# Kernel optimization log

Hardware: AMD Instinct MI355X
Metric: run time of the kernel (lower is better)

## Reference

```python
import jax, jax.numpy as jnp
from jax import lax
import numpy as np

T, B, H, D = 1024, 32, 8, 32
YD = 3 * D + 1
IN = H * D


def setup_inputs() -> dict:
    key = jax.random.key(0)
    ks = jax.random.split(key, 6)
    std = 1.0 / np.sqrt(D)
    return {
        "h": jax.random.normal(ks[0], (T, B, IN), jnp.float32),
        "W_y": (jax.random.normal(ks[1], (1, H, D, YD), jnp.float32) * std),
        "W_q": (jax.random.normal(ks[2], (1, H, D, D), jnp.float32) * std),
        "W_k": (jax.random.normal(ks[3], (1, H, D, D), jnp.float32) * std),
        "w_b": (jax.random.normal(ks[4], (1, H, D, 4), jnp.float32) * std),
        "W_out": (jax.random.normal(ks[5], (IN, IN), jnp.float32) / np.sqrt(IN)),
        "state_W_y": jnp.zeros((B, H, D, YD), jnp.float32),
        "state_W_q": jnp.zeros((B, H, D, D), jnp.float32),
        "state_W_k": jnp.zeros((B, H, D, D), jnp.float32),
        "state_w_b": jnp.zeros((B, H, D, 4), jnp.float32),
        "fast_weights": jnp.zeros((B, H, D, D), jnp.float32),
    }


def _srwm(x, Wy0, Wq0, Wk0, wb0):
    # Self-referential weight matrix (self_ref_v1): x time-major (T,B,H,D).
    def step(carry, x_t):
        Wy, Wq, Wk, wb = carry
        y = jnp.einsum('bhd,bhde->bhe', x_t, Wy)                      # output with W_{t-1}
        q = jax.nn.softmax(jnp.einsum('bhd,bhde->bhe', x_t, Wq), -1)
        k = jax.nn.softmax(jnp.einsum('bhd,bhde->bhe', x_t, Wk), -1)
        beta = jax.nn.sigmoid(jnp.einsum('bhd,bhde->bhe', x_t, wb))   # (B,H,4) learning rates
        def upd(M, b_i):
            vq = jnp.einsum('bhd,bhde->bhe', q, M)
            vk = jnp.einsum('bhd,bhde->bhe', k, M)
            return M + b_i[..., None, None] * k[..., :, None] * (vq - vk)[..., None, :]
        Wy = upd(Wy, beta[..., 0])
        Wq = upd(Wq, beta[..., 1])
        Wk = upd(Wk, beta[..., 2])
        wb = upd(wb, beta[..., 3])
        return (Wy, Wq, Wk, wb), y

    _, ys = lax.scan(step, (Wy0, Wq0, Wk0, wb0), x)
    return ys  # (T,B,H,YD)


def _fast_weight_memory(q, k, v, beta, F0):
    # Delta-rule fast weight memory; q,k,v (T,B,H,D), beta (T,B,H,1), F0 (B,H,D,D).
    def step(F, qkvb):
        q_t, k_t, v_t, b_t = qkvb
        v_old = jnp.einsum('bhd,bhde->bhe', k_t, F)
        F = F + b_t[..., None] * k_t[..., :, None] * (v_t - v_old)[..., None, :]
        out_t = jnp.einsum('bhd,bhde->bhe', q_t, F)
        return F, out_t

    F_fin, out = lax.scan(step, F0, (q, k, v, beta))
    return out, F_fin  # out: (T,B,H,D)


def reference(h, W_y, W_q, W_k, w_b, W_out,
              state_W_y, state_W_q, state_W_k, state_w_b, fast_weights):
    x = jax.nn.softmax(h.reshape(T, B, H, D), axis=-1)   # phi(x)
    Wy0 = state_W_y + W_y
    Wq0 = state_W_q + W_q
    Wk0 = state_W_k + W_k
    wb0 = state_w_b + w_b
    fast_qkvb = _srwm(x, Wy0, Wq0, Wk0, wb0)             # (T,B,H,3D+1)
    fq, fk, fv, fb = jnp.split(fast_qkvb, (D, 2 * D, 3 * D), axis=-1)
    fq = jax.nn.softmax(fq, -1)
    fk = jax.nn.softmax(fk, -1)
    fb = jax.nn.sigmoid(fb)
    out, _ = _fast_weight_memory(fq, fk, fv, fb, fast_weights)
    out = out.reshape(T, B, H * D)
    out = out @ W_out.T                                  # out_linear (no bias), dropout=0
    return h + out
```

## Files before the change

kernel.cpp:

```cpp
#include <hip/hip_runtime.h>
#include <cstdint>

#define TT  1024
#define BB  32
#define HH  8
#define DD  32
#define YDN 97
#define INN 256
#define BH  (BB*HH)

typedef float v2f __attribute__((ext_vector_type(2)));
typedef float v4f __attribute__((ext_vector_type(4)));

#define PK(acc, a, b) (acc) = __builtin_elementwise_fma((a), (b), (acc))

__device__ __forceinline__ void bar_lds() {
    asm volatile("s_waitcnt lgkmcnt(0)\n\ts_barrier" ::: "memory");
}

template<int C>
__device__ __forceinline__ float dppf(float x) {
    return __int_as_float(__builtin_amdgcn_update_dpp(
        0, __float_as_int(x), C, 0xF, 0xF, true));
}
__device__ __forceinline__ float swz16(float x) {
    return __int_as_float(__builtin_amdgcn_ds_swizzle(__float_as_int(x), 0x401F));
}
__device__ __forceinline__ float xswap32(float v) {
    return __shfl_xor(v, 32, 64);
}
__device__ __forceinline__ float red_max32(float v) {
    v = fmaxf(v, dppf<0xB1>(v));
    v = fmaxf(v, dppf<0x4E>(v));
    v = fmaxf(v, dppf<0x141>(v));
    v = fmaxf(v, dppf<0x140>(v));
    v = fmaxf(v, swz16(v));
    return v;
}
__device__ __forceinline__ float red_sum32(float v) {
    v += dppf<0xB1>(v);
    v += dppf<0x4E>(v);
    v += dppf<0x141>(v);
    v += dppf<0x140>(v);
    v += swz16(v);
    return v;
}

__device__ __forceinline__ float cexp(float v) {
    return __expf(fminf(v, 60.f));
}

__device__ __forceinline__ float dot32(const v2f (&x)[16], const v2f (&w)[16]) {
    v2f a0 = {0.f, 0.f}, a1 = {0.f, 0.f};
    #pragma unroll
    for (int g = 0; g < 8; g++) {
        PK(a0, x[2*g],   w[2*g]);
        PK(a1, x[2*g+1], w[2*g+1]);
    }
    v2f s = a0 + a1;
    return s.x + s.y;
}

__device__ __forceinline__ void lds_read32x2(const float* a, const float* b,
                                             v2f (&ra)[16], v2f (&rb)[16]) {
    const v4f* ap = (const v4f*)a;
    const v4f* bp = (const v4f*)b;
    #pragma unroll
    for (int j = 0; j < 8; j++) {
        v4f x = ap[j]; ra[2*j] = x.xy; ra[2*j+1] = x.zw;
        v4f y = bp[j]; rb[2*j] = y.xy; rb[2*j+1] = y.zw;
    }
}

__global__ __launch_bounds__(256, 1) void softmax_x_kernel(
    const float* __restrict__ hg, float* __restrict__ xg)
{
    const int row  = blockIdx.x * 8 + (threadIdx.x >> 5);
    const int lane = threadIdx.x & 31;
    float v = hg[(size_t)row * DD + lane];
    float m = red_max32(v);
    float ex = __expf(v - m);
    float sm = red_sum32(ex);
    xg[(size_t)row * DD + lane] = ex * __builtin_amdgcn_rcpf(sm);
}


#define PHASE_D(TP)                                                           \
    {                                                                         \
        const v4f* q4 = (const v4f*)fq_s;                                     \
        const v4f* k4 = (const v4f*)fk_s;                                     \
        v2f fqh[8], fkh[8];                                                   \
        _Pragma("unroll")                                                     \
        for (int j = 0; j < 4; j++) {                                         \
            v4f a = q4[4*half + j];                                           \
            fqh[2*j] = a.xy; fqh[2*j+1] = a.zw;                               \
            v4f b = k4[4*half + j];                                           \
            fkh[2*j] = b.xy; fkh[2*j+1] = b.zw;                               \
        }                                                                     \
        v2f a0 = {0.f,0.f}, a1 = {0.f,0.f};                                   \
        _Pragma("unroll")                                                     \
        for (int j = 0; j < 4; j++) {                                         \
            PK(a0, fkh[2*j],   F8[2*j]);                                      \
            PK(a1, fkh[2*j+1], F8[2*j+1]);                                    \
        }                                                                     \
        v2f vt = a0 + a1;                                                     \
        float vh = vt.x + vt.y;                                               \
        float vold = vh + xswap32(vh);                                        \
        float d2s  = fb_r * (fv_r - vold);                                    \
        v2f d2 = {d2s, d2s};                                                  \
        v2f o0 = {0.f,0.f}, o1 = {0.f,0.f};                                   \
        _Pragma("unroll")                                                     \
        for (int j = 0; j < 4; j++) {                                         \
            PK(F8[2*j],   d2, fkh[2*j]);   PK(o0, fqh[2*j],   F8[2*j]);       \
            PK(F8[2*j+1], d2, fkh[2*j+1]); PK(o1, fqh[2*j+1], F8[2*j+1]);     \
        }                                                                     \
        v2f ot = o0 + o1;                                                     \
        float oh = ot.x + ot.y;                                               \
        float oo = oh + xswap32(oh);                                          \
        if (lane < DD)                                                        \
            Og[((size_t)(TP) * BH + bh) * DD + lane] = oo;                    \
    }

#define STEP(T, XC, BUF)                                                      \
  {                                                                           \
                              \
    if (wv == 3) {                                                            \
        if ((T) > 0) { PHASE_D((T)-1) }                                       \
    } else if (wv == 2) {                                                     \
        float pre = dot32(XC, row2);                                          \
        float ex  = cexp(pre);                                                \
        float sm  = red_sum32(ex);                                            \
        float nh  = ex * __builtin_amdgcn_rcpf(sm);                           \
        float oth = xswap32(nh);                                              \
        if (lane < DD) u_s[BUF][lane]      = nh - oth;                        \
        else           k_s[BUF][lane - DD] = nh;                              \
    } else if (mat >= 0) {                                                    \
        float pre = dot32(XC, row2);                                          \
        if (wv == 0)        y_s[BUF][lane] = pre;                             \
        else if (mat == 0)  y_s[BUF][64 + lane] = pre;                        \
        else                beta_s[BUF][lane - 33] =                          \
                 __builtin_amdgcn_rcpf(1.f + __expf(-pre));                   \
    }                                                                         \
    bar_lds();                                                                \
                              \
    if (wv == 3) {                                                            \
        float fpre = y_s[BUF][lane];                                          \
        float ex = cexp(fpre);                                                \
        float r  = __builtin_amdgcn_rcpf(red_sum32(ex));                      \
        float n  = ex * r;                                                    \
        if (lane < DD) fq_s[lane]      = n;                                   \
        else           fk_s[lane - DD] = n;                                   \
        fv_r = y_s[BUF][64 + (lane & 31)];                                    \
        fb_r = __builtin_amdgcn_rcpf(1.f + __expf(-y_s[BUF][96]));            \
    } else if (mat >= 0) {                                                    \
        v2f uu[16], kk[16];                                                   \
        lds_read32x2(u_s[BUF], k_s[BUF], uu, kk);                             \
        if ((T) + 2 < TT) {                      \
            const v4f* p =                                                    \
                (const v4f*)(xg + ((size_t)((T)+2)*BH + bh)*DD);              \
            _Pragma("unroll")                                                 \
            for (int g = 0; g < 8; g++) {                                     \
                v4f v = p[g];                                                 \
                XC[2*g]   = v.xy;                                             \
                XC[2*g+1] = v.zw;                                             \
            }                                                                 \
        }                                                                     \
        float du = dot32(uu, row2);                                           \
        float bs = beta_s[BUF][mat] * du;                                     \
        v2f bs2 = {bs, bs};                                                   \
        _Pragma("unroll")                                                     \
        for (int j = 0; j < 16; j++) PK(row2[j], bs2, kk[j]);                 \
    }                                                                         \
  }

__global__ __launch_bounds__(256, 1) void srwm_fwm_kernel(
    const float* __restrict__ xg,
    const float* __restrict__ Wy_g, const float* __restrict__ Wq_g,
    const float* __restrict__ Wk_g, const float* __restrict__ wb_g,
    const float* __restrict__ sWy_g, const float* __restrict__ sWq_g,
    const float* __restrict__ sWk_g, const float* __restrict__ swb_g,
    const float* __restrict__ F_g,
    float* __restrict__ Og)
{
    const int bh   = blockIdx.x;
    const int hh   = bh & 7;
    const int tid  = threadIdx.x;
    const int wv   = tid >> 6;
    const int lane = tid & 63;
    const int half = lane >> 5;
    const int l32  = lane & 31;

    __shared__ __align__(16) float y_s[2][104];
    __shared__ __align__(16) float u_s[2][DD];
    __shared__ __align__(16) float k_s[2][DD];
    __shared__ __align__(16) float beta_s[2][4];
    __shared__ __align__(16) float fq_s[DD];
    __shared__ __align__(16) float fk_s[DD];

    v2f row2[16];
    v2f F8[8];
    v2f XA[16], XB[16];
    float fv_r = 0.f, fb_r = 0.f;

    int mat = -1;
    if (wv == 0) mat = 0;
    else if (wv == 1) { if (lane <= 32) mat = 0; else if (lane <= 36) mat = 3; }
    else if (wv == 2) mat = (lane < 32) ? 1 : 2;

    if (wv < 3) {
        const float* wp = nullptr; const float* sp = nullptr; int str = 0;
        if (wv == 0) {
            wp = Wy_g  + (size_t)hh * DD * YDN + lane;
            sp = sWy_g + (size_t)bh * DD * YDN + lane;  str = YDN;
        } else if (wv == 1) {
            if (lane <= 32) {
                wp = Wy_g  + (size_t)hh * DD * YDN + 64 + lane;
                sp = sWy_g + (size_t)bh * DD * YDN + 64 + lane;  str = YDN;
            } else if (lane <= 36) {
                wp = wb_g  + (size_t)hh * DD * 4 + (lane - 33);
                sp = swb_g + (size_t)bh * DD * 4 + (lane - 33);  str = 4;
            }
        } else {
            if (lane < 32) {
                wp = Wq_g  + (size_t)hh * DD * DD + lane;
                sp = sWq_g + (size_t)bh * DD * DD + lane;
            } else {
                wp = Wk_g  + (size_t)hh * DD * DD + (lane - 32);
                sp = sWk_g + (size_t)bh * DD * DD + (lane - 32);
            }
            str = DD;
        }
        #pragma unroll
        for (int d = 0; d < 16; d++) {
            v2f t = {0.f, 0.f};
            if (wp) {
                t.x = wp[(2*d)   * str] + sp[(2*d)   * str];
                t.y = wp[(2*d+1) * str] + sp[(2*d+1) * str];
            }
            row2[d] = t;
        }
        const v4f* p0 = (const v4f*)(xg + (size_t)bh * DD);
        const v4f* p1 = (const v4f*)(xg + ((size_t)BH + bh) * DD);
        #pragma unroll
        for (int g = 0; g < 8; g++) {
            v4f a = p0[g], b = p1[g];
            XA[2*g] = a.xy; XA[2*g+1] = a.zw;
            XB[2*g] = b.xy; XB[2*g+1] = b.zw;
        }
    } else {
        const float* fp = F_g + (size_t)bh * DD * DD + (size_t)(16*half) * DD + l32;
        #pragma unroll
        for (int j = 0; j < 8; j++) {
            v2f t;
            t.x = fp[(2*j)   * DD];
            t.y = fp[(2*j+1) * DD];
            F8[j] = t;
        }
    }

    for (int t = 0; t < TT; t += 2) {
        STEP(t,     XA, 0)
        STEP(t + 1, XB, 1)
    }
    if (wv == 3) { PHASE_D(TT - 1) }
}

#define GM 128
#define GN 128
#define GK 16

__global__ __launch_bounds__(256, 1) void out_proj_kernel(
    const float* __restrict__ O, const float* __restrict__ W,
    const float* __restrict__ hg, float* __restrict__ outg)
{
    __shared__ float As[GK][GM + 4];
    __shared__ float Bs[GK][GN + 4];
    const int tid = threadIdx.x;
    const int tx  = tid & 15;
    const int ty  = tid >> 4;
    const int r0  = blockIdx.x * GM;
    const int c0  = blockIdx.y * GN;

    float acc[8][8];
    #pragma unroll
    for (int i = 0; i < 8; i++)
        #pragma unroll
        for (int j = 0; j < 8; j++) acc[i][j] = 0.f;

    const int am = tid >> 1;
    const int ak = (tid & 1) * 8;

    for (int k0 = 0; k0 < INN; k0 += GK) {
        float4 a0 = *(const float4*)(O + (size_t)(r0 + am) * INN + k0 + ak);
        float4 a1 = *(const float4*)(O + (size_t)(r0 + am) * INN + k0 + ak + 4);
        float4 b0 = *(const float4*)(W + (size_t)(c0 + am) * INN + k0 + ak);
        float4 b1 = *(const float4*)(W + (size_t)(c0 + am) * INN + k0 + ak + 4);
        As[ak+0][am] = a0.x; As[ak+1][am] = a0.y; As[ak+2][am] = a0.z; As[ak+3][am] = a0.w;
        As[ak+4][am] = a1.x; As[ak+5][am] = a1.y; As[ak+6][am] = a1.z; As[ak+7][am] = a1.w;
        Bs[ak+0][am] = b0.x; Bs[ak+1][am] = b0.y; Bs[ak+2][am] = b0.z; Bs[ak+3][am] = b0.w;
        Bs[ak+4][am] = b1.x; Bs[ak+5][am] = b1.y; Bs[ak+6][am] = b1.z; Bs[ak+7][am] = b1.w;
        __syncthreads();
        #pragma unroll
        for (int k = 0; k < GK; k++) {
            float4 av0 = *(const float4*)&As[k][ty * 8];
            float4 av1 = *(const float4*)&As[k][ty * 8 + 4];
            float4 bv0 = *(const float4*)&Bs[k][tx * 8];
            float4 bv1 = *(const float4*)&Bs[k][tx * 8 + 4];
            float a[8] = {av0.x, av0.y, av0.z, av0.w, av1.x, av1.y, av1.z, av1.w};
            float bb[8] = {bv0.x, bv0.y, bv0.z, bv0.w, bv1.x, bv1.y, bv1.z, bv1.w};
            #pragma unroll
            for (int i = 0; i < 8; i++)
                #pragma unroll
                for (int j = 0; j < 8; j++) acc[i][j] += a[i] * bb[j];
        }
        __syncthreads();
    }

    #pragma unroll
    for (int i = 0; i < 8; i++) {
        size_t r = (size_t)(r0 + ty * 8 + i);
        float4 h0 = *(const float4*)(hg + r * INN + c0 + tx * 8);
        float4 h1 = *(const float4*)(hg + r * INN + c0 + tx * 8 + 4);
        float4 o0, o1;
        o0.x = h0.x + acc[i][0]; o0.y = h0.y + acc[i][1];
        o0.z = h0.z + acc[i][2]; o0.w = h0.w + acc[i][3];
        o1.x = h1.x + acc[i][4]; o1.y = h1.y + acc[i][5];
        o1.z = h1.z + acc[i][6]; o1.w = h1.w + acc[i][7];
        *(float4*)(outg + r * INN + c0 + tx * 8)     = o0;
        *(float4*)(outg + r * INN + c0 + tx * 8 + 4) = o1;
    }
}

extern "C" void kernel_launch(void* const* d_in, const int* in_sizes, int n_in,
                              void* d_out, int out_size, void* d_ws, size_t ws_size,
                              hipStream_t stream)
{
    (void)in_sizes; (void)n_in; (void)out_size; (void)ws_size;

    const float* hg   = (const float*)d_in[0];
    const float* Wy   = (const float*)d_in[1];
    const float* Wq   = (const float*)d_in[2];
    const float* Wk   = (const float*)d_in[3];
    const float* wb   = (const float*)d_in[4];
    const float* Wout = (const float*)d_in[5];
    const float* sWy  = (const float*)d_in[6];
    const float* sWq  = (const float*)d_in[7];
    const float* sWk  = (const float*)d_in[8];
    const float* swb  = (const float*)d_in[9];
    const float* Fw   = (const float*)d_in[10];
    float* out = (float*)d_out;

    float* xg = (float*)d_ws;
    float* Og = xg + (size_t)TT * BB * INN;

    softmax_x_kernel<<<TT * BB * HH / 8, 256, 0, stream>>>(hg, xg);
    srwm_fwm_kernel<<<BB * HH, 256, 0, stream>>>(xg, Wy, Wq, Wk, wb,
                                                 sWy, sWq, sWk, swb, Fw, Og);
    out_proj_kernel<<<dim3(TT * BB / GM, INN / GN), 256, 0, stream>>>(Og, Wout, hg, out);
}
```

Baseline: 803.5 us.

## Restructure SRWM step to one barrier per timestep with deferred updates

Each timestep now needs one workgroup barrier instead of two. The SRWM weight-row updates for step t-1 are deferred to the start of step t. Wave 2 reads its own u/k from LDS right after writing them, without a barrier. The fast-weight softmax normalization moves into wave 3: it receives unnormalized exponentials and folds the reciprocal sums into the delta and output scaling, which removes a separate softmax phase. This shortens the serial critical path per step, at the cost of numerics that differ slightly from the reference and some subtle ordering assumptions between waves.

```diff
diff --git a/kernel.cpp b/kernel.cpp
--- a/kernel.cpp
+++ b/kernel.cpp
@@ -17,6 +17,9 @@
 __device__ __forceinline__ void bar_lds() {
     asm volatile("s_waitcnt lgkmcnt(0)\n\ts_barrier" ::: "memory");
 }
+__device__ __forceinline__ void wait_lds() {
+    asm volatile("s_waitcnt lgkmcnt(0)" ::: "memory");
+}
 
 template<int C>
 __device__ __forceinline__ float dppf(float x) {
@@ -70,6 +73,17 @@
         v4f x = ap[j]; ra[2*j] = x.xy; ra[2*j+1] = x.zw;
         v4f y = bp[j]; rb[2*j] = y.xy; rb[2*j+1] = y.zw;
     }
+}
+
+__device__ __forceinline__ void upd_row(v2f (&row2)[16], const float* u_p,
+                                        const float* k_p, float beta) {
+    v2f uu0[16], kk0[16];
+    lds_read32x2(u_p, k_p, uu0, kk0);
+    float du = dot32(uu0, row2);
+    float bs = beta * du;
+    v2f bs2 = {bs, bs};
+    #pragma unroll
+    for (int j = 0; j < 16; j++) PK(row2[j], bs2, kk0[j]);
 }
 
 __global__ __launch_bounds__(256, 1) void softmax_x_kernel(
@@ -85,18 +99,25 @@
 }
 
 
-#define PHASE_D(TP)                                                           \
+#define PHASE_D(TP, P)                                                        \
     {                                                                         \
-        const v4f* q4 = (const v4f*)fq_s;                                     \
-        const v4f* k4 = (const v4f*)fk_s;                                     \
+        const v4f* e4 = (const v4f*)exf_s[P];                                 \
         v2f fqh[8], fkh[8];                                                   \
         _Pragma("unroll")                                                     \
         for (int j = 0; j < 4; j++) {                                         \
-            v4f a = q4[4*half + j];                                           \
+            v4f a = e4[4*half + j];                                           \
             fqh[2*j] = a.xy; fqh[2*j+1] = a.zw;                               \
-            v4f b = k4[4*half + j];                                           \
+            v4f b = e4[8 + 4*half + j];                                       \
             fkh[2*j] = b.xy; fkh[2*j+1] = b.zw;                               \
         }                                                                     \
+        float fvv = yv_s[P][l32];                                            \
+        float fbp = yv_s[P][32];                                             \
+                                     \
+        v2f sq2 = {0.f,0.f}, sk2 = {0.f,0.f};                                 \
+        _Pragma("unroll")                                                     \
+        for (int j = 0; j < 8; j++) { sq2 += fqh[j]; sk2 += fkh[j]; }         \
+        float sq = sq2.x + sq2.y, sk = sk2.x + sk2.y;                         \
+                         \
         v2f a0 = {0.f,0.f}, a1 = {0.f,0.f};                                   \
         _Pragma("unroll")                                                     \
         for (int j = 0; j < 4; j++) {                                         \
@@ -105,9 +126,14 @@
         }                                                                     \
         v2f vt = a0 + a1;                                                     \
         float vh = vt.x + vt.y;                                               \
-        float vold = vh + xswap32(vh);                                        \
-        float d2s  = fb_r * (fv_r - vold);                                    \
-        v2f d2 = {d2s, d2s};                                                  \
+        float voldr = vh + xswap32(vh);                                       \
+        float sqt = sq + xswap32(sq);                                         \
+        float skt = sk + xswap32(sk);                                         \
+        float rrfq = __builtin_amdgcn_rcpf(sqt);                              \
+        float rrfk = __builtin_amdgcn_rcpf(skt);                              \
+        float fbv  = __builtin_amdgcn_rcpf(1.f + __expf(-fbp));               \
+        float sup  = fbv * (fvv - rrfk * voldr) * rrfk;                       \
+        v2f d2 = {sup, sup};                                                  \
         v2f o0 = {0.f,0.f}, o1 = {0.f,0.f};                                   \
         _Pragma("unroll")                                                     \
         for (int j = 0; j < 4; j++) {                                         \
@@ -116,61 +142,62 @@
         }                                                                     \
         v2f ot = o0 + o1;                                                     \
         float oh = ot.x + ot.y;                                               \
-        float oo = oh + xswap32(oh);                                          \
+        float oo = (oh + xswap32(oh)) * rrfq;                                 \
         if (lane < DD)                                                        \
             Og[((size_t)(TP) * BH + bh) * DD + lane] = oo;                    \
     }
 
-#define STEP(T, XC, BUF)                                                      \
+#define PREFETCH(T, XC)                                                       \
+    if ((T) + 2 < TT) {                                                       \
+        const v4f* p = (const v4f*)(xg + ((size_t)((T)+2)*BH + bh)*DD);       \
+        _Pragma("unroll")                                                     \
+        for (int g = 0; g < 8; g++) {                                         \
+            v4f v = p[g];                                                     \
+            XC[2*g]   = v.xy;                                                 \
+            XC[2*g+1] = v.zw;                                                 \
+        }                                                                     \
+    }
+
+#define STEP_I(T, XC, P, PM)                                                  \
   {                                                                           \
-                              \
-    if (wv == 3) {                                                            \
-        if ((T) > 0) { PHASE_D((T)-1) }                                       \
-    } else if (wv == 2) {                                                     \
+    if (wv == 2) {                                                            \
+        if ((T) > 0) {                                                        \
+            float bb = (lane < 32) ? beta_s[PM][1] : beta_s[PM][2];           \
+            float du = dot32(uu, row2);                                       \
+            float bs = bb * du;                                               \
+            v2f bs2 = {bs, bs};                                               \
+            _Pragma("unroll")                                                 \
+            for (int j = 0; j < 16; j++) PK(row2[j], bs2, kk[j]);             \
+        }                                                                     \
         float pre = dot32(XC, row2);                                          \
         float ex  = cexp(pre);                                                \
         float sm  = red_sum32(ex);                                            \
         float nh  = ex * __builtin_amdgcn_rcpf(sm);                           \
         float oth = xswap32(nh);                                              \
-        if (lane < DD) u_s[BUF][lane]      = nh - oth;                        \
-        else           k_s[BUF][lane - DD] = nh;                              \
-    } else if (mat >= 0) {                                                    \
+        if (lane < DD) u_s[P][lane]      = nh - oth;                          \
+        else           k_s[P][lane - DD] = nh;                                \
+        wait_lds();         \
+        lds_read32x2(u_s[P], k_s[P], uu, kk);                                 \
+        PREFETCH(T, XC)                                                       \
+    } else if (wv == 0) {                                                     \
+        if ((T) > 0) upd_row(row2, u_s[PM], k_s[PM], beta_s[PM][0]);          \
         float pre = dot32(XC, row2);                                          \
-        if (wv == 0)        y_s[BUF][lane] = pre;                             \
-        else if (mat == 0)  y_s[BUF][64 + lane] = pre;                        \
-        else                beta_s[BUF][lane - 33] =                          \
+        exf_s[P][lane] = cexp(pre);                                           \
+        PREFETCH(T, XC)                                                       \
+    } else if (wv == 1) {                                                     \
+        if ((T) > 0) {                                                        \
+            float bb = (lane <= 32) ? beta_s[PM][0] : beta_s[PM][3];          \
+            upd_row(row2, u_s[PM], k_s[PM], bb);                              \
+        }                                                                     \
+        float pre = dot32(XC, row2);                                          \
+        if (lane <= DD)      yv_s[P][lane] = pre;                             \
+        else if (lane <= 36) beta_s[P][lane - 33] =                           \
                  __builtin_amdgcn_rcpf(1.f + __expf(-pre));                   \
+        PREFETCH(T, XC)                                                       \
+    } else {                                                                  \
+        if ((T) > 0) { PHASE_D((T)-1, PM) }                                   \
     }                                                                         \
     bar_lds();                                                                \
-                              \
-    if (wv == 3) {                                                            \
-        float fpre = y_s[BUF][lane];                                          \
-        float ex = cexp(fpre);                                                \
-        float r  = __builtin_amdgcn_rcpf(red_sum32(ex));                      \
-        float n  = ex * r;                                                    \
-        if (lane < DD) fq_s[lane]      = n;                                   \
-        else           fk_s[lane - DD] = n;                                   \
-        fv_r = y_s[BUF][64 + (lane & 31)];                                    \
-        fb_r = __builtin_amdgcn_rcpf(1.f + __expf(-y_s[BUF][96]));            \
-    } else if (mat >= 0) {                                                    \
-        v2f uu[16], kk[16];                                                   \
-        lds_read32x2(u_s[BUF], k_s[BUF], uu, kk);                             \
-        if ((T) + 2 < TT) {                      \
-            const v4f* p =                                                    \
-                (const v4f*)(xg + ((size_t)((T)+2)*BH + bh)*DD);              \
-            _Pragma("unroll")                                                 \
-            for (int g = 0; g < 8; g++) {                                     \
-                v4f v = p[g];                                                 \
-                XC[2*g]   = v.xy;                                             \
-                XC[2*g+1] = v.zw;                                             \
-            }                                                                 \
-        }                                                                     \
-        float du = dot32(uu, row2);                                           \
-        float bs = beta_s[BUF][mat] * du;                                     \
-        v2f bs2 = {bs, bs};                                                   \
-        _Pragma("unroll")                                                     \
-        for (int j = 0; j < 16; j++) PK(row2[j], bs2, kk[j]);                 \
-    }                                                                         \
   }
 
 __global__ __launch_bounds__(256, 1) void srwm_fwm_kernel(
@@ -190,22 +217,16 @@
     const int half = lane >> 5;
     const int l32  = lane & 31;
 
-    __shared__ __align__(16) float y_s[2][104];
     __shared__ __align__(16) float u_s[2][DD];
     __shared__ __align__(16) float k_s[2][DD];
+    __shared__ __align__(16) float exf_s[2][64];
+    __shared__ __align__(16) float yv_s[2][36];
     __shared__ __align__(16) float beta_s[2][4];
-    __shared__ __align__(16) float fq_s[DD];
-    __shared__ __align__(16) float fk_s[DD];
 
     v2f row2[16];
     v2f F8[8];
+    v2f uu[16], kk[16];
     v2f XA[16], XB[16];
-    float fv_r = 0.f, fb_r = 0.f;
-
-    int mat = -1;
-    if (wv == 0) mat = 0;
-    else if (wv == 1) { if (lane <= 32) mat = 0; else if (lane <= 36) mat = 3; }
-    else if (wv == 2) mat = (lane < 32) ? 1 : 2;
 
     if (wv < 3) {
         const float* wp = nullptr; const float* sp = nullptr; int str = 0;
@@ -259,10 +280,10 @@
     }
 
     for (int t = 0; t < TT; t += 2) {
-        STEP(t,     XA, 0)
-        STEP(t + 1, XB, 1)
-    }
-    if (wv == 3) { PHASE_D(TT - 1) }
+        STEP_I(t,     XA, 0, 1)
+        STEP_I(t + 1, XB, 1, 0)
+    }
+    if (wv == 3) { PHASE_D(TT - 1, 1) }
 }
 
 #define GM 128
```

Measured after the change: 652.4 us. -18.8%, faster.
